# Performance work log

Hardware: AMD Instinct MI355X
Metric: run time of the kernel (lower is better)

The kernel has to match this reference:

```python
import jax, jax.numpy as jnp
import numpy as np

N0, N1, N2 = 100000, 400000, 100000
EU0, EU1, EB1, EB2 = 1600000, 1200000, 800000, 300000
D, H = 64, 64  # layer_dim, hidden
BN_EPS = 1e-5


def _bn(x, g, b):
    # BatchNorm1d in training mode (batch statistics, biased variance)
    m = jnp.mean(x, axis=0)
    v = jnp.mean((x - m) ** 2, axis=0)
    return (x - m) * jax.lax.rsqrt(v + BN_EPS) * g + b


def _mlp(x, W1, b1, g1, be1, W2, b2, g2, be2):
    # Linear -> BN -> ReLU -> Linear -> BN -> ReLU
    h = jax.nn.relu(_bn(x @ W1 + b1, g1, be1))
    return jax.nn.relu(_bn(h @ W2 + b2, g2, be2))


def setup_inputs() -> dict:
    key = jax.random.key(0)
    ks = jax.random.split(key, 16)
    s = 0.1  # weight init scale
    inp = {
        'x0': jax.random.normal(ks[0], (N0, D), jnp.float32),
        'x1': jax.random.normal(ks[1], (N1, D), jnp.float32),
        'x2': jax.random.normal(ks[2], (N2, D), jnp.float32),
        'up_index0': jax.random.randint(ks[3], (2, EU0), 0, N0, jnp.int32),
        'up_index1': jax.random.randint(ks[4], (2, EU1), 0, N1, jnp.int32),
        'bnd_src1': jax.random.randint(ks[5], (EB1,), 0, N0, jnp.int32),
        'bnd_dst1': jax.random.randint(ks[6], (EB1,), 0, N1, jnp.int32),
        'bnd_src2': jax.random.randint(ks[7], (EB2,), 0, N1, jnp.int32),
        'bnd_dst2': jax.random.randint(ks[8], (EB2,), 0, N2, jnp.int32),
        'up_W1': jax.random.normal(ks[9], (3, D, H), jnp.float32) * s,
        'up_b1': jnp.zeros((3, H), jnp.float32),
        'up_g1': jnp.ones((3, H), jnp.float32),
        'up_be1': jnp.zeros((3, H), jnp.float32),
        'up_W2': jax.random.normal(ks[10], (3, H, H), jnp.float32) * s,
        'up_b2': jnp.zeros((3, H), jnp.float32),
        'up_g2': jnp.ones((3, H), jnp.float32),
        'up_be2': jnp.zeros((3, H), jnp.float32),
        'bd_W1': jax.random.normal(ks[11], (3, D, H), jnp.float32) * s,
        'bd_b1': jnp.zeros((3, H), jnp.float32),
        'bd_g1': jnp.ones((3, H), jnp.float32),
        'bd_be1': jnp.zeros((3, H), jnp.float32),
        'bd_W2': jax.random.normal(ks[12], (3, H, H), jnp.float32) * s,
        'bd_b2': jnp.zeros((3, H), jnp.float32),
        'bd_g2': jnp.ones((3, H), jnp.float32),
        'bd_be2': jnp.zeros((3, H), jnp.float32),
        'cmb_W': jax.random.normal(ks[13], (3, 2 * H, H), jnp.float32) * s,
        'cmb_b': jnp.zeros((3, H), jnp.float32),
        'cmb_g': jnp.ones((3, H), jnp.float32),
        'cmb_be': jnp.zeros((3, H), jnp.float32),
        'eps': jnp.zeros((3,), jnp.float32),  # eps1 per dim (eps2 unused in forward)
    }
    return inp


def reference(x0, x1, x2, up_index0, up_index1, bnd_src1, bnd_dst1, bnd_src2, bnd_dst2,
              up_W1, up_b1, up_g1, up_be1, up_W2, up_b2, up_g2, up_be2,
              bd_W1, bd_b1, bd_g1, bd_be1, bd_W2, bd_b2, bd_g2, bd_be2,
              cmb_W, cmb_b, cmb_g, cmb_be, eps):
    seg = jax.ops.segment_sum

    def level(d, x, agg_up, agg_bd):
        z = (1.0 + eps[d]) * x
        out_up = _mlp(agg_up + z, up_W1[d], up_b1[d], up_g1[d], up_be1[d],
                      up_W2[d], up_b2[d], up_g2[d], up_be2[d])
        out_bd = _mlp(agg_bd + z, bd_W1[d], bd_b1[d], bd_g1[d], bd_be1[d],
                      bd_W2[d], bd_b2[d], bd_g2[d], bd_be2[d])
        cat = jnp.concatenate([out_up, out_bd], axis=-1)
        return jax.nn.relu(_bn(cat @ cmb_W[d] + cmb_b[d], cmb_g[d], cmb_be[d]))

    # dim 0: upper adjacency only (no boundaries for nodes)
    agg_up0 = seg(x0[up_index0[0]], up_index0[1], num_segments=N0)
    out0 = level(0, x0, agg_up0, jnp.zeros_like(x0))

    # dim 1: upper adjacency (via 2-cells) + node boundaries (boundary_attr = x0)
    agg_up1 = seg(x1[up_index1[0]], up_index1[1], num_segments=N1)
    agg_bd1 = seg(x0[bnd_src1], bnd_dst1, num_segments=N1)
    out1 = level(1, x1, agg_up1, agg_bd1)

    # dim 2: edge boundaries only (boundary_attr = x1), no upper adjacency
    agg_bd2 = seg(x1[bnd_src2], bnd_dst2, num_segments=N2)
    out2 = level(2, x2, jnp.zeros_like(x2), agg_bd2)

    return (out0, out1, out2)
```

## Files before the change

### kernel.cpp

```cpp
#include <hip/hip_runtime.h>
#include <cstdint>
#include <cstddef>


using bfrag = __attribute__((ext_vector_type(8))) short;
using f32x4 = __attribute__((ext_vector_type(4))) float;
using u4v   = __attribute__((ext_vector_type(4))) unsigned int;
using f4v   = __attribute__((ext_vector_type(4))) float;

__device__ __forceinline__ unsigned short f2bf(float f) {
    unsigned int u = __float_as_uint(f);
    u += 0x7FFFu + ((u >> 16) & 1u);
    return (unsigned short)(u >> 16);
}
__device__ __forceinline__ float bf2f(unsigned int h) {
    return __uint_as_float(h << 16);
}


__global__ __launch_bounds__(256) void hist_ranged_k(
    const int* __restrict__ d0, const int* __restrict__ d1,
    const int* __restrict__ d2, const int* __restrict__ d3,
    int E0, int E1, int E2, int E3,
    int o0, int o1, int o2, int o3,
    int* __restrict__ cnt, int NT)
{
    const int pass = blockIdx.x & 7;
    const int W = (NT + 7) >> 3;
    const int lo = pass * W;
    int hi = lo + W; if (hi > NT) hi = NT;
    const int ET = E0 + E1 + E2 + E3;
    const int nsub = gridDim.x >> 3;
    for (int e = (blockIdx.x >> 3) * 256 + threadIdx.x; e < ET; e += nsub * 256) {
        int g;
        if (e < E0) g = o0 + d0[e];
        else if (e < E0 + E1) g = o1 + d1[e - E0];
        else if (e < E0 + E1 + E2) g = o2 + d2[e - E0 - E1];
        else g = o3 + d3[e - E0 - E1 - E2];
        if (g >= lo && g < hi) atomicAdd(&cnt[g], 1);
    }
}

__global__ __launch_bounds__(256) void fill_ranged_k(
    const int* __restrict__ s0, const int* __restrict__ d0,
    const int* __restrict__ s1, const int* __restrict__ d1,
    const int* __restrict__ s2, const int* __restrict__ d2,
    const int* __restrict__ s3, const int* __restrict__ d3,
    int E0, int E1, int E2, int E3,
    int o0, int o1, int o2, int o3,
    int* __restrict__ cur, int* __restrict__ esrc, int NT)
{
    const int pass = blockIdx.x & 7;
    const int W = (NT + 7) >> 3;
    const int lo = pass * W;
    int hi = lo + W; if (hi > NT) hi = NT;
    const int ET = E0 + E1 + E2 + E3;
    const int nsub = gridDim.x >> 3;
    for (int e = (blockIdx.x >> 3) * 256 + threadIdx.x; e < ET; e += nsub * 256) {
        int g; const int* sp; int ei;
        if (e < E0) { g = o0 + d0[e]; sp = s0; ei = e; }
        else if (e < E0 + E1) { ei = e - E0; g = o1 + d1[ei]; sp = s1; }
        else if (e < E0 + E1 + E2) { ei = e - E0 - E1; g = o2 + d2[ei]; sp = s2; }
        else { ei = e - E0 - E1 - E2; g = o3 + d3[ei]; sp = s3; }
        if (g >= lo && g < hi) {
            int pos = atomicAdd(&cur[g], 1);
            esrc[pos] = sp[ei];
        }
    }
}

__global__ __launch_bounds__(256) void scanA_k(int* __restrict__ a,
                                               int* __restrict__ bsum, int n) {
    __shared__ int ts[256];
    int tid = threadIdx.x;
    int base = blockIdx.x * 2048 + tid * 8;
    int v[8]; int s = 0;
    #pragma unroll
    for (int i = 0; i < 8; ++i) { v[i] = (base + i < n) ? a[base + i] : 0; s += v[i]; }
    ts[tid] = s;
    __syncthreads();
    for (int off = 1; off < 256; off <<= 1) {
        int t = (tid >= off) ? ts[tid - off] : 0;
        __syncthreads();
        ts[tid] += t;
        __syncthreads();
    }
    int run = ts[tid] - s;
    #pragma unroll
    for (int i = 0; i < 8; ++i) {
        if (base + i < n) { int o = v[i]; a[base + i] = run; run += o; }
    }
    if (tid == 255) bsum[blockIdx.x] = ts[255];
}

__global__ __launch_bounds__(512) void scanB_k(int* __restrict__ bsum, int nb) {
    __shared__ int ls[512];
    int tid = threadIdx.x;
    int v = (tid < nb) ? bsum[tid] : 0;
    ls[tid] = v;
    __syncthreads();
    for (int off = 1; off < 512; off <<= 1) {
        int t = (tid >= off) ? ls[tid - off] : 0;
        __syncthreads();
        ls[tid] += t;
        __syncthreads();
    }
    if (tid < nb) bsum[tid] = ls[tid] - v;
}

__global__ __launch_bounds__(256) void scanC_k(int* __restrict__ a,
                                               const int* __restrict__ bsum, int n) {
    int base = blockIdx.x * 2048 + threadIdx.x * 8;
    int add = bsum[blockIdx.x];
    #pragma unroll
    for (int i = 0; i < 8; ++i)
        if (base + i < n) a[base + i] += add;
}


__global__ __launch_bounds__(256) void wprep_k(
    const float* __restrict__ upW1, const float* __restrict__ upW2,
    const float* __restrict__ bdW1, const float* __restrict__ bdW2,
    const float* __restrict__ cmbW, unsigned short* __restrict__ wT)
{
    int id = blockIdx.x;
    int d = id / 5, j = id % 5;
    const float* src; int K = 64;
    if (j == 0)      src = upW1 + (size_t)d * 4096;
    else if (j == 1) src = upW2 + (size_t)d * 4096;
    else if (j == 2) src = bdW1 + (size_t)d * 4096;
    else if (j == 3) src = bdW2 + (size_t)d * 4096;
    else           { src = cmbW + (size_t)d * 8192; K = 128; }
    unsigned short* dst = wT + (size_t)d * 24576 + (j < 4 ? j * 4096 : 16384);
    for (int e = threadIdx.x; e < K * 64; e += 256) {
        int k = e >> 6, n = e & 63;
        dst[n * K + k] = f2bf(src[e]);
    }
}


struct SegP {
    const int* curU; const int* curB;
    const float* xsU; const float* xsB;
    const float* xself;
    const unsigned short* wTU; const unsigned short* wTB;
    const float* biasU; const float* biasB;
    unsigned short* outU; unsigned short* outB;
    float* statsU; float* statsB;
    int N; int blk0; int eBaseU; int eBaseB; int epsIdx;
};
struct PairArgs { SegP s[3]; const int* esrc; const float* epsP; };

__global__ __launch_bounds__(256) void gemm_pair_k(PairArgs A)
{
    __shared__ unsigned short sIn[64][72];
    __shared__ unsigned short sW[64][72];
    __shared__ float sBias[64];
    __shared__ float sRedS[4][64];
    __shared__ float sRedQ[4][64];

    int si = 0;
    if ((int)blockIdx.x >= A.s[1].blk0) si = 1;
    if ((int)blockIdx.x >= A.s[2].blk0) si = 2;
    const SegP S = A.s[si];
    const int* esrc = A.esrc;

    const int tid = threadIdx.x;
    const int row0 = ((int)blockIdx.x - S.blk0) * 64;
    const int N = S.N;
    const float sx = 1.0f + A.epsP[S.epsIdx];

    const int wv = tid >> 6, l = tid & 63, l15 = l & 15, quad = l >> 4;
    const int grp = tid >> 4, lane = tid & 15;
    const int r0g = row0 + grp * 4;

    float axU[4], ayU[4], azU[4], awU[4];
    float axB[4], ayB[4], azB[4], awB[4];
    #pragma unroll
    for (int rr = 0; rr < 4; ++rr) {
        int gr = r0g + rr;
        float4 xv = {0.f, 0.f, 0.f, 0.f};
        if (gr < N)
            xv = *(const float4*)(S.xself + (size_t)gr * 64 + lane * 4);
        axU[rr] = sx * xv.x; ayU[rr] = sx * xv.y;
        azU[rr] = sx * xv.z; awU[rr] = sx * xv.w;
        axB[rr] = axU[rr]; ayB[rr] = ayU[rr];
        azB[rr] = azU[rr]; awB[rr] = awU[rr];
    }

    auto gatherAcc = [&](const int* cur, int eBase, const float* xs,
                         float (&ax)[4], float (&ay)[4], float (&az)[4],
                         float (&aw)[4]) {
        if (!cur) return;
        int beg[4], deg[4];
        #pragma unroll
        for (int rr = 0; rr < 4; ++rr) {
            int gr = r0g + rr; int b = 0, d = 0;
            if (gr < N) {
                b = (gr == 0) ? eBase : cur[gr - 1];
                d = cur[gr] - b;
            }
            beg[rr] = b; deg[rr] = d;
        }
        #pragma unroll
        for (int rr = 0; rr < 4; ++rr) {
            for (int base = 0; base < deg[rr]; base += 16) {
                int take = deg[rr] - base; if (take > 16) take = 16;
                int idxl = 0;
                if (lane < take) idxl = esrc[beg[rr] + base + lane];
                for (int j0 = 0; j0 < take; j0 += 4) {
                    float4 v0 = {0,0,0,0}, v1 = {0,0,0,0};
                    float4 v2 = {0,0,0,0}, v3 = {0,0,0,0};
                    int si2 = __shfl(idxl, j0, 16);
                    v0 = *(const float4*)(xs + (size_t)si2 * 64 + lane * 4);
                    if (j0 + 1 < take) {
                        si2 = __shfl(idxl, j0 + 1, 16);
                        v1 = *(const float4*)(xs + (size_t)si2 * 64 + lane * 4);
                    }
                    if (j0 + 2 < take) {
                        si2 = __shfl(idxl, j0 + 2, 16);
                        v2 = *(const float4*)(xs + (size_t)si2 * 64 + lane * 4);
                    }
                    if (j0 + 3 < take) {
                        si2 = __shfl(idxl, j0 + 3, 16);
                        v3 = *(const float4*)(xs + (size_t)si2 * 64 + lane * 4);
                    }
                    ax[rr] += (v0.x + v1.x) + (v2.x + v3.x);
                    ay[rr] += (v0.y + v1.y) + (v2.y + v3.y);
                    az[rr] += (v0.z + v1.z) + (v2.z + v3.z);
                    aw[rr] += (v0.w + v1.w) + (v2.w + v3.w);
                }
            }
        }
    };
    gatherAcc(S.curU, S.eBaseU, S.xsU, axU, ayU, azU, awU);
    gatherAcc(S.curB, S.eBaseB, S.xsB, axB, ayB, azB, awB);

    #pragma unroll
    for (int br = 0; br < 2; ++br) {
        if (br) __syncthreads();
        const unsigned short* wTp = br ? S.wTB : S.wTU;
        const float* biasp = br ? S.biasB : S.biasU;
        unsigned short* outp = br ? S.outB : S.outU;
        float* statsp = br ? S.statsB : S.statsU;

        if (tid < 64) sBias[tid] = biasp[tid];
        {
            ushort4 pk;
            #pragma unroll
            for (int rr = 0; rr < 4; ++rr) {
                float x_ = br ? axB[rr] : axU[rr];
                float y_ = br ? ayB[rr] : ayU[rr];
                float z_ = br ? azB[rr] : azU[rr];
                float w_ = br ? awB[rr] : awU[rr];
                pk.x = f2bf(x_); pk.y = f2bf(y_);
                pk.z = f2bf(z_); pk.w = f2bf(w_);
                *(ushort4*)&sIn[grp * 4 + rr][lane * 4] = pk;
            }
        }
        #pragma unroll
        for (int it = 0; it < 2; ++it) {
            int id = tid + it * 256;
            int nr = id >> 3, c8 = id & 7;
            uint4 w = *(const uint4*)(wTp + (size_t)nr * 64 + c8 * 8);
            *(uint4*)&sW[nr][c8 * 8] = w;
        }
        __syncthreads();

        bfrag a0 = *(const bfrag*)&sIn[16 * wv + l15][quad * 8];
        bfrag a1 = *(const bfrag*)&sIn[16 * wv + l15][32 + quad * 8];
        f32x4 acc[4] = {};
        #pragma unroll
        for (int c = 0; c < 4; ++c) {
            bfrag b0 = *(const bfrag*)&sW[16 * c + l15][quad * 8];
            bfrag b1 = *(const bfrag*)&sW[16 * c + l15][32 + quad * 8];
            acc[c] = __builtin_amdgcn_mfma_f32_16x16x32_bf16(a0, b0, acc[c], 0, 0, 0);
            acc[c] = __builtin_amdgcn_mfma_f32_16x16x32_bf16(a1, b1, acc[c], 0, 0, 0);
        }
        __syncthreads();

        float psv[4], pqv[4];
        #pragma unroll
        for (int c = 0; c < 4; ++c) {
            int col = 16 * c + l15;
            float b = sBias[col];
            float ps = 0.f, pq = 0.f;
            #pragma unroll
            for (int r4 = 0; r4 < 4; ++r4) {
                int lr = 16 * wv + quad * 4 + r4;
                float v = acc[c][r4] + b;
                sIn[lr][col] = f2bf(v);
                if (row0 + lr < N) { ps += v; pq += v * v; }
            }
            psv[c] = ps; pqv[c] = pq;
        }
        #pragma unroll
        for (int c = 0; c < 4; ++c) {
            float ps = psv[c], pq = pqv[c];
            ps += __shfl_xor(ps, 16, 64); pq += __shfl_xor(pq, 16, 64);
            ps += __shfl_xor(ps, 32, 64); pq += __shfl_xor(pq, 32, 64);
            if (l < 16) { sRedS[wv][16 * c + l] = ps; sRedQ[wv][16 * c + l] = pq; }
        }
        __syncthreads();

        #pragma unroll
        for (int it = 0; it < 2; ++it) {
            int id = tid + it * 256;
            int r = id >> 3, c8 = id & 7;
            if (row0 + r < N) {
                u4v w = *(const u4v*)&sIn[r][c8 * 8];
                __builtin_nontemporal_store(
                    w, (u4v*)(outp + (size_t)(row0 + r) * 64 + c8 * 8));
            }
        }
        if (tid < 64) {
            float s = sRedS[0][tid] + sRedS[1][tid] + sRedS[2][tid] + sRedS[3][tid];
            float q = sRedQ[0][tid] + sRedQ[1][tid] + sRedQ[2][tid] + sRedQ[3][tid];
            unsafeAtomicAdd(&statsp[tid], s);
            unsafeAtomicAdd(&statsp[64 + tid], q);
        }
    }
}


struct SegG {
    const unsigned short* in0; const unsigned short* in1;
    const float* st0; const float* g0; const float* be0;
    const float* st1; const float* g1; const float* be1;
    const unsigned short* wT; const float* bias;
    unsigned short* out; float* ostats;
    int N; int blk0;
};
struct GemmArgs { SegG s[6]; int nseg; };

__global__ __launch_bounds__(256) void gemm_bn_multi_k(int mode, GemmArgs A)
{
    __shared__ unsigned short sIn[64][72];
    __shared__ unsigned short sW[64][72];
    __shared__ float sCoef[4][64];
    __shared__ float sBias[64];
    __shared__ float sRedS[4][64];
    __shared__ float sRedQ[4][64];

    int si = 0;
    #pragma unroll
    for (int i = 1; i < 6; ++i)
        if (i < A.nseg && (int)blockIdx.x >= A.s[i].blk0) si = i;
    const SegG S = A.s[si];

    const int tid = threadIdx.x;
    const int row0 = ((int)blockIdx.x - S.blk0) * 64;
    const int N = S.N;
    const float Nf = (float)N;

    if (tid < 64) {
        sBias[tid] = S.bias[tid];
        float s = S.st0[tid], sq = S.st0[64 + tid];
        float m = s / Nf, v = sq / Nf - m * m;
        float a = S.g0[tid] * rsqrtf(v + 1e-5f);
        sCoef[0][tid] = a; sCoef[1][tid] = S.be0[tid] - a * m;
    } else if (tid < 128 && mode == 2) {
        int k = tid - 64;
        float s = S.st1[k], sq = S.st1[64 + k];
        float m = s / Nf, v = sq / Nf - m * m;
        float a = S.g1[k] * rsqrtf(v + 1e-5f);
        sCoef[2][k] = a; sCoef[3][k] = S.be1[k] - a * m;
    }
    __syncthreads();

    f32x4 acc[4] = {};
    const int K = (mode == 2) ? 128 : 64;
    const int nch = (mode == 2) ? 2 : 1;
    const int wv = tid >> 6, l = tid & 63, l15 = l & 15, quad = l >> 4;

    for (int ch = 0; ch < nch; ++ch) {
        if (ch) __syncthreads();
        const unsigned short* base = ch ? S.in1 : S.in0;
        const int ci = ch * 2;
        #pragma unroll
        for (int it = 0; it < 2; ++it) {
            int id = tid + it * 256;
            int r = id >> 3, c8 = id & 7;
            int gr = row0 + r;
            uint4 pk = {0u, 0u, 0u, 0u};
            if (gr < N) {
                uint4 raw = *(const uint4*)(base + (size_t)gr * 64 + c8 * 8);
                unsigned int rw[4] = {raw.x, raw.y, raw.z, raw.w};
                unsigned int ow[4];
                #pragma unroll
                for (int q2 = 0; q2 < 4; ++q2) {
                    int col = c8 * 8 + q2 * 2;
                    float v0 = fmaxf(fmaf(sCoef[ci][col], bf2f(rw[q2] & 0xFFFFu),
                                          sCoef[ci + 1][col]), 0.f);
                    float v1 = fmaxf(fmaf(sCoef[ci][col + 1], bf2f(rw[q2] >> 16),
                                          sCoef[ci + 1][col + 1]), 0.f);
                    ow[q2] = (unsigned int)f2bf(v0) | ((unsigned int)f2bf(v1) << 16);
                }
                pk.x = ow[0]; pk.y = ow[1]; pk.z = ow[2]; pk.w = ow[3];
            }
            *(uint4*)&sIn[r][c8 * 8] = pk;
        }
        #pragma unroll
        for (int it = 0; it < 2; ++it) {
            int id = tid + it * 256;
            int nr = id >> 3, c8 = id & 7;
            uint4 w = *(const uint4*)(S.wT + (size_t)nr * K + ch * 64 + c8 * 8);
            *(uint4*)&sW[nr][c8 * 8] = w;
        }
        __syncthreads();
        bfrag a0 = *(const bfrag*)&sIn[16 * wv + l15][quad * 8];
        bfrag a1 = *(const bfrag*)&sIn[16 * wv + l15][32 + quad * 8];
        #pragma unroll
        for (int c = 0; c < 4; ++c) {
            bfrag b0 = *(const bfrag*)&sW[16 * c + l15][quad * 8];
            bfrag b1 = *(const bfrag*)&sW[16 * c + l15][32 + quad * 8];
            acc[c] = __builtin_amdgcn_mfma_f32_16x16x32_bf16(a0, b0, acc[c], 0, 0, 0);
            acc[c] = __builtin_amdgcn_mfma_f32_16x16x32_bf16(a1, b1, acc[c], 0, 0, 0);
        }
    }

    float psv[4], pqv[4];
    #pragma unroll
    for (int c = 0; c < 4; ++c) {
        int col = 16 * c + l15;
        float b = sBias[col];
        float ps = 0.f, pq = 0.f;
        #pragma unroll
        for (int r = 0; r < 4; ++r) {
            int grow = row0 + 16 * wv + quad * 4 + r;
            if (grow < N) {
                float v = acc[c][r] + b;
                S.out[(size_t)grow * 64 + col] = f2bf(v);
                ps += v; pq += v * v;
            }
        }
        psv[c] = ps; pqv[c] = pq;
    }
    #pragma unroll
    for (int c = 0; c < 4; ++c) {
        float ps = psv[c], pq = pqv[c];
        ps += __shfl_xor(ps, 16, 64); pq += __shfl_xor(pq, 16, 64);
        ps += __shfl_xor(ps, 32, 64); pq += __shfl_xor(pq, 32, 64);
        if (l < 16) { sRedS[wv][16 * c + l] = ps; sRedQ[wv][16 * c + l] = pq; }
    }
    __syncthreads();
    if (tid < 64) {
        float s = sRedS[0][tid] + sRedS[1][tid] + sRedS[2][tid] + sRedS[3][tid];
        float q = sRedQ[0][tid] + sRedQ[1][tid] + sRedQ[2][tid] + sRedQ[3][tid];
        unsafeAtomicAdd(&S.ostats[tid], s);
        unsafeAtomicAdd(&S.ostats[64 + tid], q);
    }
}


struct SegA {
    const unsigned short* in; const float* st; const float* g; const float* be;
    float* out; int N; int blk0;
};
struct ApplyArgs { SegA s[2]; int nseg; };

__global__ __launch_bounds__(256) void bn_relu_apply_multi_k(ApplyArgs A)
{
    __shared__ float sa[64], sc[64];
    int si = 0;
    if (A.nseg > 1 && (int)blockIdx.x >= A.s[1].blk0) si = 1;
    const SegA S = A.s[si];
    int tid = threadIdx.x;
    if (tid < 64) {
        float s = S.st[tid], sq = S.st[64 + tid];
        float m = s / (float)S.N, v = sq / (float)S.N - m * m;
        float a = S.g[tid] * rsqrtf(v + 1e-5f);
        sa[tid] = a; sc[tid] = S.be[tid] - a * m;
    }
    __syncthreads();
    int idx = ((int)blockIdx.x - S.blk0) * 256 + tid;
    if (idx < S.N * 8) {
        int r = idx >> 3, c8 = idx & 7;
        uint4 raw = *(const uint4*)(S.in + (size_t)r * 64 + c8 * 8);
        unsigned int rw[4] = {raw.x, raw.y, raw.z, raw.w};
        float o[8];
        #pragma unroll
        for (int q = 0; q < 4; ++q) {
            int col = c8 * 8 + q * 2;
            o[q * 2 + 0] = fmaxf(fmaf(sa[col + 0], bf2f(rw[q] & 0xFFFFu), sc[col + 0]), 0.f);
            o[q * 2 + 1] = fmaxf(fmaf(sa[col + 1], bf2f(rw[q] >> 16), sc[col + 1]), 0.f);
        }
        f4v o0 = {o[0], o[1], o[2], o[3]}, o1 = {o[4], o[5], o[6], o[7]};
        __builtin_nontemporal_store(o0, (f4v*)(S.out + (size_t)r * 64 + c8 * 8));
        __builtin_nontemporal_store(o1, (f4v*)(S.out + (size_t)r * 64 + c8 * 8 + 4));
    }
}

extern "C" void kernel_launch(void* const* d_in, const int* in_sizes, int n_in,
                              void* d_out, int out_size, void* d_ws, size_t ws_size,
                              hipStream_t stream) {
    (void)n_in; (void)out_size; (void)ws_size;
    const float* x0 = (const float*)d_in[0];
    const float* x1 = (const float*)d_in[1];
    const float* x2 = (const float*)d_in[2];
    const int* up_index0 = (const int*)d_in[3];
    const int* up_index1 = (const int*)d_in[4];
    const int* bnd_src1  = (const int*)d_in[5];
    const int* bnd_dst1  = (const int*)d_in[6];
    const int* bnd_src2  = (const int*)d_in[7];
    const int* bnd_dst2  = (const int*)d_in[8];
    const float* up_W1 = (const float*)d_in[9];
    const float* up_b1 = (const float*)d_in[10];
    const float* up_g1 = (const float*)d_in[11];
    const float* up_be1= (const float*)d_in[12];
    const float* up_W2 = (const float*)d_in[13];
    const float* up_b2 = (const float*)d_in[14];
    const float* up_g2 = (const float*)d_in[15];
    const float* up_be2= (const float*)d_in[16];
    const float* bd_W1 = (const float*)d_in[17];
    const float* bd_b1 = (const float*)d_in[18];
    const float* bd_g1 = (const float*)d_in[19];
    const float* bd_be1= (const float*)d_in[20];
    const float* bd_W2 = (const float*)d_in[21];
    const float* bd_b2 = (const float*)d_in[22];
    const float* bd_g2 = (const float*)d_in[23];
    const float* bd_be2= (const float*)d_in[24];
    const float* cmb_W = (const float*)d_in[25];
    const float* cmb_b = (const float*)d_in[26];
    const float* cmb_g = (const float*)d_in[27];
    const float* cmb_be= (const float*)d_in[28];
    const float* epsP  = (const float*)d_in[29];

    const int EU0 = in_sizes[3] / 2, EU1 = in_sizes[4] / 2;
    const int EB1 = in_sizes[5],     EB2 = in_sizes[7];
    const int n0 = in_sizes[0] / 64, n1 = in_sizes[1] / 64, n2 = in_sizes[2] / 64;
    const int nMax02 = (n0 > n2) ? n0 : n2;

    float* outP = (float*)d_out;

    unsigned short* bufU = (unsigned short*)d_ws;
    unsigned short* bufB = bufU + (size_t)n1 * 64;
    float* stats = (float*)(bufB + (size_t)nMax02 * 64);
    int*   bsum  = (int*)(stats + 15 * 128);
    unsigned short* wT = (unsigned short*)(bsum + 1024);

    const int NT  = n0 + 2 * n1 + n2;
    const int oU0 = 0, oU1 = n0, oB1 = n0 + n1, oB2 = n0 + 2 * n1;
    const int eU0 = 0, eU1 = EU0, eB1 = EU0 + EU1, eB2 = EU0 + EU1 + EB1;
    int* curAll  = (int*)(outP + (size_t)(n0 + n1) * 64);
    int* esrcAll = curAll + NT;

    unsigned short* hU0 = bufB;
    unsigned short* hB0 = (unsigned short*)outP;
    unsigned short* hU2 = (unsigned short*)outP + (size_t)n0 * 64;
    unsigned short* hU1 = bufU;
    unsigned short* hB1 = (unsigned short*)(outP + (size_t)n0 * 64);
    unsigned short* hB2 = (unsigned short*)(outP + (size_t)n0 * 64) + (size_t)n1 * 64;

    hipMemsetAsync(stats, 0, 15 * 128 * sizeof(float), stream);
    wprep_k<<<15, 256, 0, stream>>>(up_W1, up_W2, bd_W1, bd_W2, cmb_W, wT);

    hipMemsetAsync(curAll, 0, (size_t)NT * sizeof(int), stream);
    hist_ranged_k<<<2048, 256, 0, stream>>>(
        up_index0 + EU0, up_index1 + EU1, bnd_dst1, bnd_dst2,
        EU0, EU1, EB1, EB2, oU0, oU1, oB1, oB2, curAll, NT);
    int nbScan = (NT + 2047) / 2048;
    scanA_k<<<nbScan, 256, 0, stream>>>(curAll, bsum, NT);
    scanB_k<<<1, 512, 0, stream>>>(bsum, nbScan);
    scanC_k<<<nbScan, 256, 0, stream>>>(curAll, bsum, NT);
    fill_ranged_k<<<2048, 256, 0, stream>>>(
        up_index0, up_index0 + EU0, up_index1, up_index1 + EU1,
        bnd_src1, bnd_dst1, bnd_src2, bnd_dst2,
        EU0, EU1, EB1, EB2, oU0, oU1, oB1, oB2, curAll, esrcAll, NT);

    auto S  = [&](int d, int i) { return stats + (size_t)(d * 5 + i) * 128; };
    auto WTf = [&](int d, int j) { return wT + (size_t)d * 24576 + (j < 4 ? j * 4096 : 16384); };

    const int nb0 = (n0 + 63) / 64, nb1 = (n1 + 63) / 64, nb2 = (n2 + 63) / 64;

    {
        PairArgs A{}; A.esrc = esrcAll; A.epsP = epsP;
        A.s[0] = { curAll + oU0, nullptr, x0, nullptr, x0,
                   WTf(0,0), WTf(0,2), up_b1 + 0, bd_b1 + 0,
                   hU0, hB0, S(0,0), S(0,2), n0, 0, eU0, 0, 0 };
        A.s[1] = { curAll + oU1, curAll + oB1, x1, x0, x1,
                   WTf(1,0), WTf(1,2), up_b1 + 64, bd_b1 + 64,
                   hU1, hB1, S(1,0), S(1,2), n1, nb0, eU1, eB1, 1 };
        A.s[2] = { nullptr, curAll + oB2, nullptr, x1, x2,
                   WTf(2,0), WTf(2,2), up_b1 + 128, bd_b1 + 128,
                   hU2, hB2, S(2,0), S(2,2), n2, nb0 + nb1, 0, eB2, 2 };
        gemm_pair_k<<<nb0 + nb1 + nb2, 256, 0, stream>>>(A);
    }

    {
        GemmArgs A{}; A.nseg = 6;
        auto& s = A.s;
        s[0] = { hU0, nullptr, S(0,0), up_g1 + 0, up_be1 + 0,
                 nullptr, nullptr, nullptr,
                 WTf(0,1), up_b2 + 0, hU0, S(0,1), n0, 0 };
        s[1] = { hB0, nullptr, S(0,2), bd_g1 + 0, bd_be1 + 0,
                 nullptr, nullptr, nullptr,
                 WTf(0,3), bd_b2 + 0, hB0, S(0,3), n0, nb0 };
        s[2] = { hU1, nullptr, S(1,0), up_g1 + 64, up_be1 + 64,
                 nullptr, nullptr, nullptr,
                 WTf(1,1), up_b2 + 64, hU1, S(1,1), n1, 2*nb0 };
        s[3] = { hB1, nullptr, S(1,2), bd_g1 + 64, bd_be1 + 64,
                 nullptr, nullptr, nullptr,
                 WTf(1,3), bd_b2 + 64, hB1, S(1,3), n1, 2*nb0 + nb1 };
        s[4] = { hU2, nullptr, S(2,0), up_g1 + 128, up_be1 + 128,
                 nullptr, nullptr, nullptr,
                 WTf(2,1), up_b2 + 128, hU2, S(2,1), n2, 2*nb0 + 2*nb1 };
        s[5] = { hB2, nullptr, S(2,2), bd_g1 + 128, bd_be1 + 128,
                 nullptr, nullptr, nullptr,
                 WTf(2,3), bd_b2 + 128, hB2, S(2,3), n2, 2*nb0 + 2*nb1 + nb2 };
        gemm_bn_multi_k<<<2*nb0 + 2*nb1 + 2*nb2, 256, 0, stream>>>(1, A);
    }

    {
        GemmArgs A{}; A.nseg = 3;
        auto& s = A.s;
        s[0] = { hU0, hB0, S(0,1), up_g2 + 0, up_be2 + 0,
                 S(0,3), bd_g2 + 0, bd_be2 + 0,
                 WTf(0,4), cmb_b + 0, hU0, S(0,4), n0, 0 };
        s[1] = { hU1, hB1, S(1,1), up_g2 + 64, up_be2 + 64,
                 S(1,3), bd_g2 + 64, bd_be2 + 64,
                 WTf(1,4), cmb_b + 64, hU1, S(1,4), n1, nb0 };
        s[2] = { hU2, hB2, S(2,1), up_g2 + 128, up_be2 + 128,
                 S(2,3), bd_g2 + 128, bd_be2 + 128,
                 WTf(2,4), cmb_b + 128, hU2, S(2,4), n2, nb0 + nb1 };
        gemm_bn_multi_k<<<nb0 + nb1 + nb2, 256, 0, stream>>>(2, A);
    }

    {
        ApplyArgs A{}; A.nseg = 1;
        A.s[0] = { hU2, S(2,4), cmb_g + 128, cmb_be + 128,
                   outP + (size_t)(n0 + n1) * 64, n2, 0 };
        bn_relu_apply_multi_k<<<(n2 * 8 + 255) / 256, 256, 0, stream>>>(A);
    }
    {
        ApplyArgs A{}; A.nseg = 2;
        int ab0 = (n0 * 8 + 255) / 256;
        A.s[0] = { hU0, S(0,4), cmb_g + 0, cmb_be + 0, outP, n0, 0 };
        A.s[1] = { hU1, S(1,4), cmb_g + 64, cmb_be + 64,
                   outP + (size_t)n0 * 64, n1, ab0 };
        bn_relu_apply_multi_k<<<ab0 + (n1 * 8 + 255) / 256, 256, 0, stream>>>(A);
    }
}
```

Baseline: 1.590 ms.

## Pre-partition edges into 8 destination buckets before histogram and CSR fill

Before the histogram, a counting pass, a scan and a scatter write each edge's (dst, src) into a buffer bucketed by the destination range. The histogram and fill kernels then read only their bucket instead of rescanning all edges eight times with a range filter. This removes the 8x redundant reads of the index arrays in exchange for three extra kernels and one write and read of the partitioned buffer. The partition buffer is placed in the output region and relies on it being large enough.

```diff
diff --git a/kernel.cpp b/kernel.cpp
--- a/kernel.cpp
+++ b/kernel.cpp
@@ -18,54 +18,151 @@
 }
 
 
-__global__ __launch_bounds__(256) void hist_ranged_k(
+__global__ __launch_bounds__(256) void part_count_k(
     const int* __restrict__ d0, const int* __restrict__ d1,
     const int* __restrict__ d2, const int* __restrict__ d3,
     int E0, int E1, int E2, int E3,
     int o0, int o1, int o2, int o3,
-    int* __restrict__ cnt, int NT)
+    int* __restrict__ bcnt, int NT)
 {
-    const int pass = blockIdx.x & 7;
+    __shared__ int c8[8];
+    const int tid = threadIdx.x;
+    if (tid < 8) c8[tid] = 0;
+    __syncthreads();
     const int W = (NT + 7) >> 3;
-    const int lo = pass * W;
-    int hi = lo + W; if (hi > NT) hi = NT;
     const int ET = E0 + E1 + E2 + E3;
-    const int nsub = gridDim.x >> 3;
-    for (int e = (blockIdx.x >> 3) * 256 + threadIdx.x; e < ET; e += nsub * 256) {
-        int g;
-        if (e < E0) g = o0 + d0[e];
-        else if (e < E0 + E1) g = o1 + d1[e - E0];
-        else if (e < E0 + E1 + E2) g = o2 + d2[e - E0 - E1];
-        else g = o3 + d3[e - E0 - E1 - E2];
-        if (g >= lo && g < hi) atomicAdd(&cnt[g], 1);
-    }
-}
-
-__global__ __launch_bounds__(256) void fill_ranged_k(
+    for (int base_e = blockIdx.x * 256; base_e < ET; base_e += gridDim.x * 256) {
+        int e = base_e + tid;
+        int k = -1;
+        if (e < ET) {
+            int g;
+            if (e < E0) g = o0 + __builtin_nontemporal_load(&d0[e]);
+            else if (e < E0 + E1) g = o1 + __builtin_nontemporal_load(&d1[e - E0]);
+            else if (e < E0 + E1 + E2) g = o2 + __builtin_nontemporal_load(&d2[e - E0 - E1]);
+            else g = o3 + __builtin_nontemporal_load(&d3[e - E0 - E1 - E2]);
+            k = g / W;
+        }
+        #pragma unroll
+        for (int kk = 0; kk < 8; ++kk) {
+            unsigned long long m = __ballot(k == kk);
+            if ((tid & 63) == 0 && m) atomicAdd(&c8[kk], (int)__popcll(m));
+        }
+    }
+    __syncthreads();
+    if (tid < 8) bcnt[tid * gridDim.x + blockIdx.x] = c8[tid];
+}
+
+__global__ __launch_bounds__(512) void part_scan_k(int* __restrict__ bcnt,
+                                                   int* __restrict__ bstart,
+                                                   int NBLK) {
+    __shared__ int ls[512];
+    const int tid = threadIdx.x;
+    const int base = tid * 8;
+    int v[8]; int s = 0;
+    #pragma unroll
+    for (int i = 0; i < 8; ++i) { v[i] = bcnt[base + i]; s += v[i]; }
+    ls[tid] = s;
+    __syncthreads();
+    for (int off = 1; off < 512; off <<= 1) {
+        int t = (tid >= off) ? ls[tid - off] : 0;
+        __syncthreads();
+        ls[tid] += t;
+        __syncthreads();
+    }
+    int run = ls[tid] - s;
+    #pragma unroll
+    for (int i = 0; i < 8; ++i) {
+        int flat = base + i;
+        if ((flat % NBLK) == 0) bstart[flat / NBLK] = run;
+        int o = v[i]; bcnt[flat] = run; run += o;
+    }
+    if (tid == 511) bstart[8] = ls[511];
+}
+
+__global__ __launch_bounds__(256) void part_scatter_k(
     const int* __restrict__ s0, const int* __restrict__ d0,
     const int* __restrict__ s1, const int* __restrict__ d1,
     const int* __restrict__ s2, const int* __restrict__ d2,
     const int* __restrict__ s3, const int* __restrict__ d3,
     int E0, int E1, int E2, int E3,
     int o0, int o1, int o2, int o3,
-    int* __restrict__ cur, int* __restrict__ esrc, int NT)
+    const int* __restrict__ bcnt,
+    int* __restrict__ dstB, int* __restrict__ srcB, int NT)
+{
+    __shared__ int cur8[8];
+    const int tid = threadIdx.x;
+    if (tid < 8) cur8[tid] = bcnt[tid * gridDim.x + blockIdx.x];
+    __syncthreads();
+    const int W = (NT + 7) >> 3;
+    const int ET = E0 + E1 + E2 + E3;
+    const int lane = tid & 63;
+    for (int base_e = blockIdx.x * 256; base_e < ET; base_e += gridDim.x * 256) {
+        int e = base_e + tid;
+        int g = 0, src = 0, k = -1;
+        if (e < ET) {
+            if (e < E0) {
+                g = o0 + __builtin_nontemporal_load(&d0[e]);
+                src = __builtin_nontemporal_load(&s0[e]);
+            } else if (e < E0 + E1) {
+                int ei = e - E0;
+                g = o1 + __builtin_nontemporal_load(&d1[ei]);
+                src = __builtin_nontemporal_load(&s1[ei]);
+            } else if (e < E0 + E1 + E2) {
+                int ei = e - E0 - E1;
+                g = o2 + __builtin_nontemporal_load(&d2[ei]);
+                src = __builtin_nontemporal_load(&s2[ei]);
+            } else {
+                int ei = e - E0 - E1 - E2;
+                g = o3 + __builtin_nontemporal_load(&d3[ei]);
+                src = __builtin_nontemporal_load(&s3[ei]);
+            }
+            k = g / W;
+        }
+        int pos = 0;
+        #pragma unroll
+        for (int kk = 0; kk < 8; ++kk) {
+            unsigned long long m = __ballot(k == kk);
+            if (m == 0ull) continue;
+            if (k == kk) {
+                int leader = (int)__ffsll(m) - 1;
+                int bse = 0;
+                if (lane == leader) bse = atomicAdd(&cur8[kk], (int)__popcll(m));
+                bse = __shfl(bse, leader, 64);
+                pos = bse + (int)__popcll(m & ((1ull << lane) - 1ull));
+            }
+        }
+        if (e < ET) { dstB[pos] = g; srcB[pos] = src; }
+    }
+}
+
+__global__ __launch_bounds__(256) void hist_b_k(
+    const int* __restrict__ dstB, const int* __restrict__ bstart,
+    int* __restrict__ cnt)
 {
     const int pass = blockIdx.x & 7;
-    const int W = (NT + 7) >> 3;
-    const int lo = pass * W;
-    int hi = lo + W; if (hi > NT) hi = NT;
-    const int ET = E0 + E1 + E2 + E3;
+    const int lo = bstart[pass], hi = bstart[pass + 1];
     const int nsub = gridDim.x >> 3;
-    for (int e = (blockIdx.x >> 3) * 256 + threadIdx.x; e < ET; e += nsub * 256) {
-        int g; const int* sp; int ei;
-        if (e < E0) { g = o0 + d0[e]; sp = s0; ei = e; }
-        else if (e < E0 + E1) { ei = e - E0; g = o1 + d1[ei]; sp = s1; }
-        else if (e < E0 + E1 + E2) { ei = e - E0 - E1; g = o2 + d2[ei]; sp = s2; }
-        else { ei = e - E0 - E1 - E2; g = o3 + d3[ei]; sp = s3; }
-        if (g >= lo && g < hi) {
-            int pos = atomicAdd(&cur[g], 1);
-            esrc[pos] = sp[ei];
-        }
+    for (int i = lo + (blockIdx.x >> 3) * 256 + threadIdx.x; i < hi;
+         i += nsub * 256) {
+        int g = __builtin_nontemporal_load(&dstB[i]);
+        atomicAdd(&cnt[g], 1);
+    }
+}
+
+__global__ __launch_bounds__(256) void fill_b_k(
+    const int* __restrict__ dstB, const int* __restrict__ srcB,
+    const int* __restrict__ bstart,
+    int* __restrict__ cur, int* __restrict__ esrc)
+{
+    const int pass = blockIdx.x & 7;
+    const int lo = bstart[pass], hi = bstart[pass + 1];
+    const int nsub = gridDim.x >> 3;
+    for (int i = lo + (blockIdx.x >> 3) * 256 + threadIdx.x; i < hi;
+         i += nsub * 256) {
+        int g = __builtin_nontemporal_load(&dstB[i]);
+        int s = __builtin_nontemporal_load(&srcB[i]);
+        int pos = atomicAdd(&cur[g], 1);
+        esrc[pos] = s;
     }
 }
 
@@ -537,13 +634,19 @@
     unsigned short* bufB = bufU + (size_t)n1 * 64;
     float* stats = (float*)(bufB + (size_t)nMax02 * 64);
     int*   bsum  = (int*)(stats + 15 * 128);
-    unsigned short* wT = (unsigned short*)(bsum + 1024);
+    int*   bcnt  = bsum + 1024;
+    int*   bstart= bcnt + 4096;
+    unsigned short* wT = (unsigned short*)(bstart + 16);
 
     const int NT  = n0 + 2 * n1 + n2;
+    const int ETT = EU0 + EU1 + EB1 + EB2;
     const int oU0 = 0, oU1 = n0, oB1 = n0 + n1, oB2 = n0 + 2 * n1;
     const int eU0 = 0, eU1 = EU0, eB1 = EU0 + EU1, eB2 = EU0 + EU1 + EB1;
     int* curAll  = (int*)(outP + (size_t)(n0 + n1) * 64);
     int* esrcAll = curAll + NT;
+
+    int* dstB = (int*)(outP + (size_t)n0 * 64);
+    int* srcB = dstB + ETT;
 
     unsigned short* hU0 = bufB;
     unsigned short* hB0 = (unsigned short*)outP;
@@ -556,17 +659,20 @@
     wprep_k<<<15, 256, 0, stream>>>(up_W1, up_W2, bd_W1, bd_W2, cmb_W, wT);
 
     hipMemsetAsync(curAll, 0, (size_t)NT * sizeof(int), stream);
-    hist_ranged_k<<<2048, 256, 0, stream>>>(
+    part_count_k<<<512, 256, 0, stream>>>(
         up_index0 + EU0, up_index1 + EU1, bnd_dst1, bnd_dst2,
-        EU0, EU1, EB1, EB2, oU0, oU1, oB1, oB2, curAll, NT);
+        EU0, EU1, EB1, EB2, oU0, oU1, oB1, oB2, bcnt, NT);
+    part_scan_k<<<1, 512, 0, stream>>>(bcnt, bstart, 512);
+    part_scatter_k<<<512, 256, 0, stream>>>(
+        up_index0, up_index0 + EU0, up_index1, up_index1 + EU1,
+        bnd_src1, bnd_dst1, bnd_src2, bnd_dst2,
+        EU0, EU1, EB1, EB2, oU0, oU1, oB1, oB2, bcnt, dstB, srcB, NT);
+    hist_b_k<<<2048, 256, 0, stream>>>(dstB, bstart, curAll);
     int nbScan = (NT + 2047) / 2048;
     scanA_k<<<nbScan, 256, 0, stream>>>(curAll, bsum, NT);
     scanB_k<<<1, 512, 0, stream>>>(bsum, nbScan);
     scanC_k<<<nbScan, 256, 0, stream>>>(curAll, bsum, NT);
-    fill_ranged_k<<<2048, 256, 0, stream>>>(
-        up_index0, up_index0 + EU0, up_index1, up_index1 + EU1,
-        bnd_src1, bnd_dst1, bnd_src2, bnd_dst2,
-        EU0, EU1, EB1, EB2, oU0, oU1, oB1, oB2, curAll, esrcAll, NT);
+    fill_b_k<<<2048, 256, 0, stream>>>(dstB, srcB, bstart, curAll, esrcAll);
 
     auto S  = [&](int d, int i) { return stats + (size_t)(d * 5 + i) * 128; };
     auto WTf = [&](int d, int j) { return wT + (size_t)d * 24576 + (j < 4 ? j * 4096 : 16384); };
```

Result: slower. 1.632 ms (+2.6%).
